# Kernel tuning notes

Measured on AMD Instinct MI355X. Metric: run time of the kernel, lower is better.

## Reference

```python
import jax, jax.numpy as jnp
import numpy as np

D = 32            # dims[0] == dims[1] (modes per register)
K = 8             # kernel_size (filter interferometer modes)
STRIDE = 8        # stride (== kernel_size -> block-diagonal register)
N_BLOCKS = (D - K) // STRIDE + 1          # filters per register = 4
N_PHI = K * (K - 1) // 2                  # Reck triangle: one Ry BS per crossing = 28
BATCH = 16


def _filter_unitary(phi):
    """K-mode Reck-triangle interferometer of BS.Ry(theta=-2*phi) gates.
    Each gate mixes adjacent modes (j-1, j) with the real rotation
    [[cos phi, sin phi], [-sin phi, cos phi]]. Returns real [K, K] orthogonal."""
    U = jnp.eye(K, dtype=phi.dtype)
    idx = 0
    for i in range(1, K):
        for j in range(i, 0, -1):
            c, s = jnp.cos(phi[idx]), jnp.sin(phi[idx])
            r0 = c * U[j - 1] + s * U[j]
            r1 = -s * U[j - 1] + c * U[j]
            U = U.at[j - 1].set(r0).at[j].set(r1)
            idx += 1
    return U


def _register_unitary(phi):
    """D-mode register: the SAME filter unitary (shared params) placed every
    STRIDE modes; identity on any leftover modes. Block-diagonal [D, D]."""
    uf = _filter_unitary(phi)
    U = jnp.eye(D, dtype=phi.dtype)
    for b in range(N_BLOCKS):
        o = b * STRIDE
        U = U.at[o:o + K, o:o + K].set(uf)
    return U


def setup_inputs() -> dict:
    key = jax.random.key(0)
    k1, k2, k3 = jax.random.split(key, 3)
    two_pi = jnp.float32(2.0 * np.pi)
    return {
        "rho": jax.random.normal(k1, (BATCH, D * D, D * D), dtype=jnp.float32),
        "phi_x": two_pi * jax.random.uniform(k2, (N_PHI,), dtype=jnp.float32),
        "phi_y": two_pi * jax.random.uniform(k3, (N_PHI,), dtype=jnp.float32),
    }


def reference(rho, phi_x, phi_y):
    # u = kron(u_x, u_y) : [D^2, D^2] real orthogonal (BS circuit => real)
    u = jnp.kron(_register_unitary(phi_x), _register_unitary(phi_y))
    # new_rho = u @ rho @ u^dagger ; real => dagger is transpose
    u_rho = jnp.einsum('ij,bjk->bik', u, rho)   # [b, D^2, D^2]
    return u_rho @ u.T
```

## Files before the change

### kernel.cpp

```cpp
#include <hip/hip_runtime.h>
#include <hip/hip_bf16.h>
#include <math.h>


typedef __attribute__((ext_vector_type(8))) short short8_t;
typedef __attribute__((ext_vector_type(4))) float f32x4;

__global__ void setup_w(const float* __restrict__ phi_x,
                        const float* __restrict__ phi_y,
                        unsigned short* __restrict__ W) {
    __shared__ float U[2][64];
    const int t = threadIdx.x;
    if (t < 2) {
        const float* phi = (t == 0) ? phi_x : phi_y;
        float Um[8][8];
#pragma unroll
        for (int i = 0; i < 8; ++i)
#pragma unroll
            for (int j = 0; j < 8; ++j) Um[i][j] = (i == j) ? 1.0f : 0.0f;
        int idx = 0;
#pragma unroll
        for (int i = 1; i < 8; ++i) {
#pragma unroll
            for (int j = i; j >= 1; --j) {
                const float c = cosf(phi[idx]);
                const float s = sinf(phi[idx]);
#pragma unroll
                for (int m = 0; m < 8; ++m) {
                    const float a = Um[j - 1][m], b = Um[j][m];
                    Um[j - 1][m] = c * a + s * b;
                    Um[j][m]     = -s * a + c * b;
                }
                ++idx;
            }
        }
#pragma unroll
        for (int i = 0; i < 8; ++i)
#pragma unroll
            for (int j = 0; j < 8; ++j) U[t][i * 8 + j] = Um[i][j];
    }
    __syncthreads();
    const int xi = t >> 3, yi = t & 7;
#pragma unroll
    for (int j = 0; j < 64; ++j) {
        const int xj = j >> 3, yj = j & 7;
        const float w = U[0][xi * 8 + xj] * U[1][yi * 8 + yj];
        __hip_bfloat16 h = __float2bfloat16(w);
        W[t * 64 + j] = *reinterpret_cast<const unsigned short*>(&h);
    }
}

__device__ __forceinline__ unsigned short bf16bits(float v) {
    __hip_bfloat16 h = __float2bfloat16(v);
    return *reinterpret_cast<const unsigned short*>(&h);
}

__global__ __launch_bounds__(256) void qconv_mfma(const float* __restrict__ rho,
                                                  const unsigned short* __restrict__ Wg,
                                                  float* __restrict__ out) {
    __shared__ __align__(16) unsigned short lds[20480];
    const int t   = threadIdx.x;
    const int wid = t >> 6;
    const int l   = t & 63;

    const int g  = blockIdx.x * 4 + wid;
    const int bj = g & 15;
    const int bi = (g >> 4) & 15;
    const int b  = g >> 8;

    const int rowb = (bi >> 2) * 256 + (bi & 3) * 8;
    const int colb = (bj >> 2) * 256 + (bj & 3) * 8;
    const size_t B0 = (size_t)b << 20;

    unsigned short* __restrict__ Tt = lds + wid * 5120;
    unsigned short* __restrict__ Pb = Tt + 4096;

    {
        const float* __restrict__ src =
            rho + B0 + (size_t)rowb * 1024 + colb + ((l >> 3) * 32 + (l & 7));
        const int l7 = l & 7;
#pragma unroll
        for (int s = 0; s < 64; ++s) {
            const float v = src[(size_t)((s >> 3) * 32 + (s & 7)) * 1024];
            Tt[l * 64 + ((((s >> 3) ^ l7) << 3) | (s & 7))] = bf16bits(v);
        }
    }

    const int ln = l & 15;
    const int q  = l >> 4;
    const int l7 = ln & 7;

#pragma unroll 1
    for (int m = 0; m < 4; ++m) {
        const short8_t a0 =
            *reinterpret_cast<const short8_t*>(Wg + ((m * 16 + ln) << 6) + (q << 3));
        const short8_t a1 =
            *reinterpret_cast<const short8_t*>(Wg + ((m * 16 + ln) << 6) + 32 + (q << 3));
        f32x4 pacc[4];
#pragma unroll
        for (int n = 0; n < 4; ++n) {
            const short8_t b0 = *reinterpret_cast<const short8_t*>(
                Tt + (n * 16 + ln) * 64 + ((q ^ l7) << 3));
            const short8_t b1 = *reinterpret_cast<const short8_t*>(
                Tt + (n * 16 + ln) * 64 + (((4 + q) ^ l7) << 3));
            f32x4 c = {0.0f, 0.0f, 0.0f, 0.0f};
            c = __builtin_amdgcn_mfma_f32_16x16x32_bf16(a0, b0, c, 0, 0, 0);
            c = __builtin_amdgcn_mfma_f32_16x16x32_bf16(a1, b1, c, 0, 0, 0);
            pacc[n] = c;
        }

#pragma unroll
        for (int n = 0; n < 4; ++n)
#pragma unroll
            for (int i = 0; i < 4; ++i) {
                const int rl = q * 4 + i;
                const int c  = n * 16 + ln;
                Pb[rl * 64 + ((((c >> 3) ^ (rl & 7)) << 3) | (c & 7))] =
                    bf16bits(pacc[n][i]);
            }

        const short8_t pa0 = *reinterpret_cast<const short8_t*>(
            Pb + ln * 64 + ((q ^ l7) << 3));
        const short8_t pa1 = *reinterpret_cast<const short8_t*>(
            Pb + ln * 64 + (((4 + q) ^ l7) << 3));
#pragma unroll
        for (int n = 0; n < 4; ++n) {
            const short8_t wb0 = *reinterpret_cast<const short8_t*>(
                Wg + ((n * 16 + ln) << 6) + (q << 3));
            const short8_t wb1 = *reinterpret_cast<const short8_t*>(
                Wg + ((n * 16 + ln) << 6) + 32 + (q << 3));
            f32x4 c = {0.0f, 0.0f, 0.0f, 0.0f};
            c = __builtin_amdgcn_mfma_f32_16x16x32_bf16(pa0, wb0, c, 0, 0, 0);
            c = __builtin_amdgcn_mfma_f32_16x16x32_bf16(pa1, wb1, c, 0, 0, 0);

#pragma unroll
            for (int i = 0; i < 4; ++i) {
                const int rr   = q * 4 + i;
                const int grow = rowb + (m * 2 + (rr >> 3)) * 32 + (rr & 7);
                const int gcol = colb + (n * 2 + (ln >> 3)) * 32 + (ln & 7);
                out[B0 + (size_t)grow * 1024 + gcol] = c[i];
            }
        }
    }
}

extern "C" void kernel_launch(void* const* d_in, const int* in_sizes, int n_in,
                              void* d_out, int out_size, void* d_ws, size_t ws_size,
                              hipStream_t stream) {
    const float* rho   = (const float*)d_in[0];
    const float* phi_x = (const float*)d_in[1];
    const float* phi_y = (const float*)d_in[2];
    float* out = (float*)d_out;
    unsigned short* W = (unsigned short*)d_ws;

    setup_w<<<1, 64, 0, stream>>>(phi_x, phi_y, W);
    qconv_mfma<<<1024, 256, 0, stream>>>(rho, W, out);
}
```

Baseline: 44.79 us.

## Restructure block-sandwich kernel for coalesced float4 loads and stores via shared LDS tiles

Each 512-thread workgroup now handles one row-block and half the columns. It loads full contiguous rho rows with float4 reads into a swizzled 64 KB bf16 LDS tile that its eight waves share, instead of each wave doing strided scalar gathers. The second MFMA is computed transposed so the output can be written as float4 vectors. The cost is 80 KB of dynamic LDS and a block-wide barrier, which lowers occupancy and adds an extra sync.

Result: faster. 43.80 us (-2.2%).

```diff
diff --git a/kernel.cpp b/kernel.cpp
--- a/kernel.cpp
+++ b/kernel.cpp
@@ -55,91 +55,112 @@
     return *reinterpret_cast<const unsigned short*>(&h);
 }
 
-__global__ __launch_bounds__(256) void qconv_mfma(const float* __restrict__ rho,
-                                                  const unsigned short* __restrict__ Wg,
-                                                  float* __restrict__ out) {
-    __shared__ __align__(16) unsigned short lds[20480];
-    const int t   = threadIdx.x;
-    const int wid = t >> 6;
-    const int l   = t & 63;
+__global__ __launch_bounds__(512) void qconv_mfma2(const float* __restrict__ rho,
+                                                   const unsigned short* __restrict__ Wg,
+                                                   float* __restrict__ out) {
+    extern __shared__ __align__(16) unsigned short L[];
+    const int t  = threadIdx.x;
+    const int w  = t >> 6;
+    const int l  = t & 63;
 
-    const int g  = blockIdx.x * 4 + wid;
-    const int bj = g & 15;
-    const int bi = (g >> 4) & 15;
-    const int b  = g >> 8;
+    const int bid = blockIdx.x;
+    const int ch  = bid & 1;
+    const int bi  = (bid >> 1) & 15;
+    const int b   = bid >> 5;
 
-    const int rowb = (bi >> 2) * 256 + (bi & 3) * 8;
-    const int colb = (bj >> 2) * 256 + (bj & 3) * 8;
-    const size_t B0 = (size_t)b << 20;
-
-    unsigned short* __restrict__ Tt = lds + wid * 5120;
-    unsigned short* __restrict__ Pb = Tt + 4096;
+    const int    rowb    = (bi >> 2) * 256 + (bi & 3) * 8;
+    const size_t B0      = (size_t)b << 20;
+    const int    colbase = ch * 512;
 
     {
-        const float* __restrict__ src =
-            rho + B0 + (size_t)rowb * 1024 + colb + ((l >> 3) * 32 + (l & 7));
-        const int l7 = l & 7;
+        float4 v[16];
 #pragma unroll
-        for (int s = 0; s < 64; ++s) {
-            const float v = src[(size_t)((s >> 3) * 32 + (s & 7)) * 1024];
-            Tt[l * 64 + ((((s >> 3) ^ l7) << 3) | (s & 7))] = bf16bits(v);
+        for (int j = 0; j < 8; ++j) {
+            const float* __restrict__ src =
+                rho + B0 + (size_t)(rowb + w * 32 + j) * 1024 + colbase;
+#pragma unroll
+            for (int k2 = 0; k2 < 2; ++k2)
+                v[j * 2 + k2] =
+                    *reinterpret_cast<const float4*>(src + 4 * l + 256 * k2);
+        }
+#pragma unroll
+        for (int j = 0; j < 8; ++j) {
+            const int rt = 8 * w + j;
+#pragma unroll
+            for (int k2 = 0; k2 < 2; ++k2) {
+                const int gc = 4 * l + 256 * k2;
+                const int u     = ((gc >> 8) << 1) | ((gc >> 4) & 1);
+                const int pcolc = ((gc >> 3) & 1) * 8 + ((gc >> 5) & 7);
+                const int chunk = pcolc ^ (rt & 15);
+                ushort4 h;
+                const float4 x = v[j * 2 + k2];
+                h.x = bf16bits(x.x); h.y = bf16bits(x.y);
+                h.z = bf16bits(x.z); h.w = bf16bits(x.w);
+                *reinterpret_cast<ushort4*>(
+                    &L[u * 8192 + rt * 128 + (chunk << 3) + (gc & 7)]) = h;
+            }
         }
     }
+    __syncthreads();
 
     const int ln = l & 15;
     const int q  = l >> 4;
-    const int l7 = ln & 7;
+    const unsigned short* __restrict__ Tp = &L[(w >> 1) * 8192];
+    unsigned short* __restrict__ Qs       = &L[32768 + w * 1024];
+    const int wc = (w & 1) * 8;
+
+    const int bx2 = 2 * ch + (w >> 2);
+    const int by2 = w & 3;
 
 #pragma unroll 1
     for (int m = 0; m < 4; ++m) {
-        const short8_t a0 =
-            *reinterpret_cast<const short8_t*>(Wg + ((m * 16 + ln) << 6) + (q << 3));
-        const short8_t a1 =
-            *reinterpret_cast<const short8_t*>(Wg + ((m * 16 + ln) << 6) + 32 + (q << 3));
-        f32x4 pacc[4];
+        const short8_t AW0 = *reinterpret_cast<const short8_t*>(
+            Wg + (16 * m + ln) * 64 + q * 8);
+        const short8_t AW1 = *reinterpret_cast<const short8_t*>(
+            Wg + (16 * m + ln) * 64 + 32 + q * 8);
+        f32x4 acc[4];
 #pragma unroll
-        for (int n = 0; n < 4; ++n) {
-            const short8_t b0 = *reinterpret_cast<const short8_t*>(
-                Tt + (n * 16 + ln) * 64 + ((q ^ l7) << 3));
-            const short8_t b1 = *reinterpret_cast<const short8_t*>(
-                Tt + (n * 16 + ln) * 64 + (((4 + q) ^ l7) << 3));
+        for (int tc = 0; tc < 4; ++tc) {
+            const int prow = 16 * tc + ln;
+            const short8_t BT0 = *reinterpret_cast<const short8_t*>(
+                Tp + prow * 128 + (((wc + 0 + q) ^ (prow & 15)) << 3));
+            const short8_t BT1 = *reinterpret_cast<const short8_t*>(
+                Tp + prow * 128 + (((wc + 4 + q) ^ (prow & 15)) << 3));
             f32x4 c = {0.0f, 0.0f, 0.0f, 0.0f};
-            c = __builtin_amdgcn_mfma_f32_16x16x32_bf16(a0, b0, c, 0, 0, 0);
-            c = __builtin_amdgcn_mfma_f32_16x16x32_bf16(a1, b1, c, 0, 0, 0);
-            pacc[n] = c;
+            c = __builtin_amdgcn_mfma_f32_16x16x32_bf16(AW0, BT0, c, 0, 0, 0);
+            c = __builtin_amdgcn_mfma_f32_16x16x32_bf16(AW1, BT1, c, 0, 0, 0);
+            acc[tc] = c;
         }
 
 #pragma unroll
-        for (int n = 0; n < 4; ++n)
+        for (int tc = 0; tc < 4; ++tc)
 #pragma unroll
             for (int i = 0; i < 4; ++i) {
-                const int rl = q * 4 + i;
-                const int c  = n * 16 + ln;
-                Pb[rl * 64 + ((((c >> 3) ^ (rl & 7)) << 3) | (c & 7))] =
-                    bf16bits(pacc[n][i]);
+                const int qrow = 4 * q + i;
+                const int qcol = 16 * tc + ln;
+                Qs[qrow * 64 + (((qcol >> 3) ^ (qrow & 7)) << 3) + (qcol & 7)] =
+                    bf16bits(acc[tc][i]);
             }
 
-        const short8_t pa0 = *reinterpret_cast<const short8_t*>(
-            Pb + ln * 64 + ((q ^ l7) << 3));
-        const short8_t pa1 = *reinterpret_cast<const short8_t*>(
-            Pb + ln * 64 + (((4 + q) ^ l7) << 3));
+        const short8_t AQ0 = *reinterpret_cast<const short8_t*>(
+            Qs + ln * 64 + (((0 + q) ^ (ln & 7)) << 3));
+        const short8_t AQ1 = *reinterpret_cast<const short8_t*>(
+            Qs + ln * 64 + (((4 + q) ^ (ln & 7)) << 3));
 #pragma unroll
-        for (int n = 0; n < 4; ++n) {
-            const short8_t wb0 = *reinterpret_cast<const short8_t*>(
-                Wg + ((n * 16 + ln) << 6) + (q << 3));
-            const short8_t wb1 = *reinterpret_cast<const short8_t*>(
-                Wg + ((n * 16 + ln) << 6) + 32 + (q << 3));
-            f32x4 c = {0.0f, 0.0f, 0.0f, 0.0f};
-            c = __builtin_amdgcn_mfma_f32_16x16x32_bf16(pa0, wb0, c, 0, 0, 0);
-            c = __builtin_amdgcn_mfma_f32_16x16x32_bf16(pa1, wb1, c, 0, 0, 0);
+        for (int tc = 0; tc < 4; ++tc) {
+            const short8_t BW0 = *reinterpret_cast<const short8_t*>(
+                Wg + (16 * tc + ln) * 64 + q * 8);
+            const short8_t BW1 = *reinterpret_cast<const short8_t*>(
+                Wg + (16 * tc + ln) * 64 + 32 + q * 8);
+            f32x4 o = {0.0f, 0.0f, 0.0f, 0.0f};
+            o = __builtin_amdgcn_mfma_f32_16x16x32_bf16(AQ0, BW0, o, 0, 0, 0);
+            o = __builtin_amdgcn_mfma_f32_16x16x32_bf16(AQ1, BW1, o, 0, 0, 0);
 
-#pragma unroll
-            for (int i = 0; i < 4; ++i) {
-                const int rr   = q * 4 + i;
-                const int grow = rowb + (m * 2 + (rr >> 3)) * 32 + (rr & 7);
-                const int gcol = colb + (n * 2 + (ln >> 3)) * 32 + (ln & 7);
-                out[B0 + (size_t)grow * 1024 + gcol] = c[i];
-            }
+            const int grow = rowb + (2 * tc + (ln >> 3)) * 32 + (ln & 7);
+            const int c0   = 16 * m + 4 * q;
+            const int gcol = bx2 * 256 + (c0 >> 3) * 32 + by2 * 8 + (c0 & 7);
+            *reinterpret_cast<float4*>(out + B0 + (size_t)grow * 1024 + gcol) =
+                make_float4(o[0], o[1], o[2], o[3]);
         }
     }
 }
@@ -154,5 +175,5 @@
     unsigned short* W = (unsigned short*)d_ws;
 
     setup_w<<<1, 64, 0, stream>>>(phi_x, phi_y, W);
-    qconv_mfma<<<1024, 256, 0, stream>>>(rho, W, out);
+    qconv_mfma2<<<512, 512, 81920, stream>>>(rho, W, out);
 }
```

## Pipeline rho tile loads with double-buffered LDS and vectorized float4 IO

Applied to the files above, without the earlier changes.

Replaces the one-tile-per-wave kernel with a 256-block kernel where each block processes four work units, loading the next unit from global memory into registers while computing the current one out of double-buffered LDS. Global loads become coalesced float4 row reads instead of strided scalar column reads, and output stores become float4. The cost is 80 KB of dynamic LDS per block, fewer blocks in flight, and block-wide barriers between stages.

New measurement: 58.82 us. +31.3%, slower.

```diff
diff --git a/kernel.cpp b/kernel.cpp
--- a/kernel.cpp
+++ b/kernel.cpp
@@ -55,93 +55,134 @@
     return *reinterpret_cast<const unsigned short*>(&h);
 }
 
-__global__ __launch_bounds__(256) void qconv_mfma(const float* __restrict__ rho,
+#define STAGE_LOAD(U)                                                          \
+    do {                                                                       \
+        const int uid_ = blockIdx.x * 4 + (U);                                 \
+        const int ch2_ = uid_ & 3, bi_ = (uid_ >> 2) & 15, bb_ = uid_ >> 6;    \
+        const float* __restrict__ sp_ =                                        \
+            rho + ((size_t)bb_ << 20) +                                        \
+            (size_t)((bi_ >> 2) * 256 + (bi_ & 3) * 8 + grow_off) * 1024 +     \
+            ch2_ * 256 + lq * 4;                                               \
+        _Pragma("unroll")                                                      \
+        for (int j = 0; j < 16; ++j)                                           \
+            v[j] = *reinterpret_cast<const float4*>(sp_ + j * 16);             \
+    } while (0)
+
+#define STAGE_WRITE(BUF)                                                       \
+    do {                                                                       \
+        _Pragma("unroll")                                                      \
+        for (int j = 0; j < 16; ++j) {                                         \
+            const int chunk_ = (((lq >> 1) * 8) + ((j >> 1) & 7)) ^ r15;       \
+            ushort4 h_;                                                        \
+            h_.x = bf16bits(v[j].x); h_.y = bf16bits(v[j].y);                  \
+            h_.z = bf16bits(v[j].z); h_.w = bf16bits(v[j].w);                  \
+            *reinterpret_cast<ushort4*>(                                       \
+                &L[(((BUF) * 2 + (j & 1)) * 64 + rr) * 128 + (chunk_ << 3) +   \
+                   (lq & 1) * 4]) = h_;                                        \
+        }                                                                      \
+    } while (0)
+
+#define COMPUTE(U, BUF)                                                        \
+    do {                                                                       \
+        const int uid_ = blockIdx.x * 4 + (U);                                 \
+        const int ch2_ = uid_ & 3, bi_ = (uid_ >> 2) & 15, bb_ = uid_ >> 6;    \
+        const size_t B0_ = (size_t)bb_ << 20;                                  \
+        const int rowb_ = (bi_ >> 2) * 256 + (bi_ & 3) * 8;                    \
+        const unsigned short* __restrict__ Tp_ =                               \
+            &L[((BUF) * 2 + (w >> 1)) * 8192];                                 \
+        unsigned short* __restrict__ Qs_ = &L[32768 + w * 1024];               \
+        const int wc_ = (w & 1) * 8;                                           \
+        const int bx2_ = ch2_, by2_ = w;                                       \
+        _Pragma("unroll")                                                      \
+        for (int m = 0; m < 4; ++m) {                                          \
+            const short8_t AW0 = *reinterpret_cast<const short8_t*>(           \
+                Wg + (16 * m + ln) * 64 + q * 8);                              \
+            const short8_t AW1 = *reinterpret_cast<const short8_t*>(           \
+                Wg + (16 * m + ln) * 64 + 32 + q * 8);                         \
+            f32x4 acc[4];                                                      \
+            _Pragma("unroll")                                                  \
+            for (int tc = 0; tc < 4; ++tc) {                                   \
+                const int prow = 16 * tc + ln;                                 \
+                const short8_t BT0 = *reinterpret_cast<const short8_t*>(       \
+                    Tp_ + prow * 128 + (((wc_ + 0 + q) ^ (prow & 15)) << 3));  \
+                const short8_t BT1 = *reinterpret_cast<const short8_t*>(       \
+                    Tp_ + prow * 128 + (((wc_ + 4 + q) ^ (prow & 15)) << 3));  \
+                f32x4 c = {0.0f, 0.0f, 0.0f, 0.0f};                            \
+                c = __builtin_amdgcn_mfma_f32_16x16x32_bf16(AW0, BT0, c, 0, 0, 0); \
+                c = __builtin_amdgcn_mfma_f32_16x16x32_bf16(AW1, BT1, c, 0, 0, 0); \
+                acc[tc] = c;                                                   \
+            }                                                                  \
+            _Pragma("unroll")                                                  \
+            for (int tc = 0; tc < 4; ++tc)                                     \
+                _Pragma("unroll")                                              \
+                for (int i = 0; i < 4; ++i) {                                  \
+                    const int qrow = 4 * q + i;                                \
+                    const int qcol = 16 * tc + ln;                             \
+                    Qs_[qrow * 64 + (((qcol >> 3) ^ (qrow & 7)) << 3) +        \
+                        (qcol & 7)] = bf16bits(acc[tc][i]);                    \
+                }                                                              \
+            const short8_t AQ0 = *reinterpret_cast<const short8_t*>(           \
+                Qs_ + ln * 64 + (((0 + q) ^ (ln & 7)) << 3));                  \
+            const short8_t AQ1 = *reinterpret_cast<const short8_t*>(           \
+                Qs_ + ln * 64 + (((4 + q) ^ (ln & 7)) << 3));                  \
+            _Pragma("unroll")                                                  \
+            for (int tc = 0; tc < 4; ++tc) {                                   \
+                const short8_t BW0 = *reinterpret_cast<const short8_t*>(       \
+                    Wg + (16 * tc + ln) * 64 + q * 8);                         \
+                const short8_t BW1 = *reinterpret_cast<const short8_t*>(       \
+                    Wg + (16 * tc + ln) * 64 + 32 + q * 8);                    \
+                f32x4 o = {0.0f, 0.0f, 0.0f, 0.0f};                            \
+                o = __builtin_amdgcn_mfma_f32_16x16x32_bf16(AQ0, BW0, o, 0, 0, 0); \
+                o = __builtin_amdgcn_mfma_f32_16x16x32_bf16(AQ1, BW1, o, 0, 0, 0); \
+                const int growg = rowb_ + (2 * tc + (ln >> 3)) * 32 + (ln & 7);\
+                const int c0    = 16 * m + 4 * q;                              \
+                const int gcol  = bx2_ * 256 + (c0 >> 3) * 32 + by2_ * 8 +     \
+                                 (c0 & 7);                                     \
+                *reinterpret_cast<float4*>(out + B0_ + (size_t)growg * 1024 +  \
+                                           gcol) =                             \
+                    make_float4(o[0], o[1], o[2], o[3]);                       \
+            }                                                                  \
+        }                                                                      \
+    } while (0)
+
+__global__ __launch_bounds__(256) void qconv_pipe(const float* __restrict__ rho,
                                                   const unsigned short* __restrict__ Wg,
                                                   float* __restrict__ out) {
-    __shared__ __align__(16) unsigned short lds[20480];
-    const int t   = threadIdx.x;
-    const int wid = t >> 6;
-    const int l   = t & 63;
+    extern __shared__ __align__(16) unsigned short L[];
+    const int t = threadIdx.x;
+    const int w = t >> 6;
+    const int l = t & 63;
 
-    const int g  = blockIdx.x * 4 + wid;
-    const int bj = g & 15;
-    const int bi = (g >> 4) & 15;
-    const int b  = g >> 8;
-
-    const int rowb = (bi >> 2) * 256 + (bi & 3) * 8;
-    const int colb = (bj >> 2) * 256 + (bj & 3) * 8;
-    const size_t B0 = (size_t)b << 20;
-
-    unsigned short* __restrict__ Tt = lds + wid * 5120;
-    unsigned short* __restrict__ Pb = Tt + 4096;
-
-    {
-        const float* __restrict__ src =
-            rho + B0 + (size_t)rowb * 1024 + colb + ((l >> 3) * 32 + (l & 7));
-        const int l7 = l & 7;
-#pragma unroll
-        for (int s = 0; s < 64; ++s) {
-            const float v = src[(size_t)((s >> 3) * 32 + (s & 7)) * 1024];
-            Tt[l * 64 + ((((s >> 3) ^ l7) << 3) | (s & 7))] = bf16bits(v);
-        }
-    }
+    const int lq = l & 3;
+    const int rr = w * 16 + (l >> 2);
+    const int r15 = rr & 15;
+    const int grow_off = (rr >> 3) * 32 + (rr & 7);
 
     const int ln = l & 15;
     const int q  = l >> 4;
-    const int l7 = ln & 7;
 
-#pragma unroll 1
-    for (int m = 0; m < 4; ++m) {
-        const short8_t a0 =
-            *reinterpret_cast<const short8_t*>(Wg + ((m * 16 + ln) << 6) + (q << 3));
-        const short8_t a1 =
-            *reinterpret_cast<const short8_t*>(Wg + ((m * 16 + ln) << 6) + 32 + (q << 3));
-        f32x4 pacc[4];
-#pragma unroll
-        for (int n = 0; n < 4; ++n) {
-            const short8_t b0 = *reinterpret_cast<const short8_t*>(
-                Tt + (n * 16 + ln) * 64 + ((q ^ l7) << 3));
-            const short8_t b1 = *reinterpret_cast<const short8_t*>(
-                Tt + (n * 16 + ln) * 64 + (((4 + q) ^ l7) << 3));
-            f32x4 c = {0.0f, 0.0f, 0.0f, 0.0f};
-            c = __builtin_amdgcn_mfma_f32_16x16x32_bf16(a0, b0, c, 0, 0, 0);
-            c = __builtin_amdgcn_mfma_f32_16x16x32_bf16(a1, b1, c, 0, 0, 0);
-            pacc[n] = c;
-        }
+    float4 v[16];
 
-#pragma unroll
-        for (int n = 0; n < 4; ++n)
-#pragma unroll
-            for (int i = 0; i < 4; ++i) {
-                const int rl = q * 4 + i;
-                const int c  = n * 16 + ln;
-                Pb[rl * 64 + ((((c >> 3) ^ (rl & 7)) << 3) | (c & 7))] =
-                    bf16bits(pacc[n][i]);
-            }
+    STAGE_LOAD(0);
+    STAGE_WRITE(0);
+    __syncthreads();
 
-        const short8_t pa0 = *reinterpret_cast<const short8_t*>(
-            Pb + ln * 64 + ((q ^ l7) << 3));
-        const short8_t pa1 = *reinterpret_cast<const short8_t*>(
-            Pb + ln * 64 + (((4 + q) ^ l7) << 3));
-#pragma unroll
-        for (int n = 0; n < 4; ++n) {
-            const short8_t wb0 = *reinterpret_cast<const short8_t*>(
-                Wg + ((n * 16 + ln) << 6) + (q << 3));
-            const short8_t wb1 = *reinterpret_cast<const short8_t*>(
-                Wg + ((n * 16 + ln) << 6) + 32 + (q << 3));
-            f32x4 c = {0.0f, 0.0f, 0.0f, 0.0f};
-            c = __builtin_amdgcn_mfma_f32_16x16x32_bf16(pa0, wb0, c, 0, 0, 0);
-            c = __builtin_amdgcn_mfma_f32_16x16x32_bf16(pa1, wb1, c, 0, 0, 0);
+    STAGE_LOAD(1);
+    COMPUTE(0, 0);
+    STAGE_WRITE(1);
+    __syncthreads();
 
-#pragma unroll
-            for (int i = 0; i < 4; ++i) {
-                const int rr   = q * 4 + i;
-                const int grow = rowb + (m * 2 + (rr >> 3)) * 32 + (rr & 7);
-                const int gcol = colb + (n * 2 + (ln >> 3)) * 32 + (ln & 7);
-                out[B0 + (size_t)grow * 1024 + gcol] = c[i];
-            }
-        }
-    }
+    STAGE_LOAD(2);
+    COMPUTE(1, 1);
+    STAGE_WRITE(0);
+    __syncthreads();
+
+    STAGE_LOAD(3);
+    COMPUTE(2, 0);
+    STAGE_WRITE(1);
+    __syncthreads();
+
+    COMPUTE(3, 1);
 }
 
 extern "C" void kernel_launch(void* const* d_in, const int* in_sizes, int n_in,
@@ -154,5 +195,5 @@
     unsigned short* W = (unsigned short*)d_ws;
 
     setup_w<<<1, 64, 0, stream>>>(phi_x, phi_y, W);
-    qconv_mfma<<<1024, 256, 0, stream>>>(rho, W, out);
+    qconv_pipe<<<256, 256, 81920, stream>>>(rho, W, out);
 }
```
